# Kernel tuning notes

Hardware: AMD Instinct MI355X
Metric: run time of the kernel (lower is better)

## Reference

```python
import jax, jax.numpy as jnp
import numpy as np
from jax import lax

B, N, DIMS, CIN, K = 32, 1024, 3, 64, 16
COUTS = [128, 128, 128]
EPS = 1e-5


def knn_idx(points, k):
    # points: [B, D, N]; pairwise_distance = -||pi - pj||^2 (torch: -xx - (-2 p^T p) - xx^T)
    xx = jnp.sum(points ** 2, axis=1)                      # [B, N]
    inner = jnp.einsum('bdn,bdm->bnm', points, points)     # [B, N, N]
    pd = 2.0 * inner - xx[:, :, None] - xx[:, None, :]     # [B, N, N]
    idx = lax.top_k(pd, k + 1)[1][:, :, 1:]                # drop self -> [B, N, K]
    return idx


def batchnorm(x, gamma, beta, axes):
    # training-mode BN: biased batch statistics per channel (last axis here)
    mean = jnp.mean(x, axis=axes, keepdims=True)
    var = jnp.mean((x - mean) ** 2, axis=axes, keepdims=True)
    return (x - mean) * lax.rsqrt(var + EPS) * gamma + beta


def reference(points, features, W0, g0, b0, W1, g1, b1, W2, g2, b2, Wsc, gsc, bsc):
    idx = knn_idx(points, K)                               # [B, N, K] int32
    feats = jnp.transpose(features, (0, 2, 1))             # [B, N, C]
    nbr = jax.vmap(lambda f, i: f[i])(feats, idx)          # [B, N, K, C]
    center = feats[:, :, None, :]                          # [B, N, 1, C]
    # torch get_graph_feature: cat((x, fts - x), dim=channel) -> [B, N, K, 2C]
    x = jnp.concatenate([jnp.broadcast_to(center, nbr.shape), nbr - center], axis=-1)
    for W, g, b in ((W0, g0, b0), (W1, g1, b1), (W2, g2, b2)):
        x = jnp.einsum('bnkc,oc->bnko', x, W)              # 1x1 conv, no bias
        x = jax.nn.relu(batchnorm(x, g, b, axes=(0, 1, 2)))
    fts = jnp.mean(x, axis=2)                              # mean over neighbors -> [B, N, Co]
    sc = jnp.einsum('bnc,oc->bno', feats, Wsc)             # shortcut 1x1 conv1d
    sc = batchnorm(sc, gsc, bsc, axes=(0, 1))
    out = jax.nn.relu(sc + fts)                            # [B, N, Co]
    return jnp.transpose(out, (0, 2, 1))                   # [B, Co, N] to match torch layout


def setup_inputs() -> dict:
    key = jax.random.key(0)
    ks = jax.random.split(key, 8)
    s = 0.05
    return {
        'points': jax.random.normal(ks[0], (B, DIMS, N), jnp.float32),
        'features': jax.random.normal(ks[1], (B, CIN, N), jnp.float32),
        'W0': jax.random.normal(ks[2], (COUTS[0], 2 * CIN), jnp.float32) * s,
        'g0': jnp.ones((COUTS[0],), jnp.float32), 'b0': jnp.zeros((COUTS[0],), jnp.float32),
        'W1': jax.random.normal(ks[3], (COUTS[1], COUTS[0]), jnp.float32) * s,
        'g1': jnp.ones((COUTS[1],), jnp.float32), 'b1': jnp.zeros((COUTS[1],), jnp.float32),
        'W2': jax.random.normal(ks[4], (COUTS[2], COUTS[1]), jnp.float32) * s,
        'g2': jnp.ones((COUTS[2],), jnp.float32), 'b2': jnp.zeros((COUTS[2],), jnp.float32),
        'Wsc': jax.random.normal(ks[5], (COUTS[2], CIN), jnp.float32) * s,
        'gsc': jnp.ones((COUTS[2],), jnp.float32), 'bsc': jnp.zeros((COUTS[2],), jnp.float32),
    }
```

## Files before the change

kernel.cpp:

```cpp
#include <hip/hip_runtime.h>


#define BB 32
#define NN 1024
#define CINC 64
#define KK 16
#define CO 128
#define NROW (BB*NN*KK)
#define NROWSC (BB*NN)

static const size_t OFF_FT   = 0;
static const size_t OFF_IDX  = 8388608;
static const size_t OFF_Y    = 10485760;
static const size_t OFF_SC   = 144703488;
static const size_t OFF_PART = 161480704;
static const size_t OFF_WB   = 165675008;
static const size_t OFF_S1   = 169869312;
static const size_t OFF_SB   = 169934848;
static const size_t WS_NEED  = 169938944;

typedef __bf16 bf16x8v __attribute__((ext_vector_type(8)));
typedef float  f32x4v  __attribute__((ext_vector_type(4)));

__device__ __forceinline__ float bl(unsigned u){ return __uint_as_float(u<<16); }
__device__ __forceinline__ float bh(unsigned u){ return __uint_as_float(u & 0xffff0000u); }
__device__ __forceinline__ unsigned short bfr(float x){
  unsigned u = __float_as_uint(x);
  u += 0x7fffu + ((u>>16)&1u);
  return (unsigned short)(u>>16);
}
__device__ __forceinline__ unsigned short b16(float x){
  return __builtin_bit_cast(unsigned short, (__bf16)x);
}

__global__ __launch_bounds__(256) void sentinel_kernel(float* __restrict__ out, int n, float v){
  int i = blockIdx.x*256 + threadIdx.x;
  if (i < n) out[i] = v;
}

__global__ __launch_bounds__(256) void prep_kernel(const float* __restrict__ f,
                                                   const float* __restrict__ pts,
                                                   const float* __restrict__ W0,
                                                   const float* __restrict__ W1,
                                                   const float* __restrict__ W2,
                                                   float* __restrict__ ft,
                                                   unsigned short* __restrict__ WB,
                                                   int* __restrict__ idxout){
  __shared__ __align__(16) char smem[34816];
  int t = threadIdx.x;
  int bid = blockIdx.x;

  if (bid < 512){
    float (*tile)[65] = (float(*)[65])smem;
    int b = bid >> 4, n0 = (bid & 15) * 64;
    for (int it=0; it<16; ++it){
      int flat = it*256 + t;
      int c = flat>>6, nl = flat&63;
      tile[c][nl] = f[(b*64 + c)*1024 + n0 + nl];
    }
    __syncthreads();
    for (int it=0; it<16; ++it){
      int flat = it*256 + t;
      int nl = flat>>6, c = flat&63;
      ft[((b<<10) + n0 + nl)*64 + c] = tile[c][nl];
    }
    return;
  }

  if (bid < 536){
    int tid = (bid - 512)*256 + t;
    int lay = tid >> 11, rem = tid & 2047;
    int fidx = rem >> 6, l = rem & 63;
    int kb = fidx >> 3, cf = fidx & 7;
    int li = l & 15, lg = l >> 4;
    const float* Ws = lay==0 ? W0 : (lay==1 ? W1 : W2);
    int o = cf*16 + li;
    unsigned short p[8];
    #pragma unroll
    for (int j=0;j<8;++j) p[j] = bfr(Ws[o*128 + kb*32 + lg*8 + j]);
    uint4 o4;
    o4.x = (unsigned)p[0] | ((unsigned)p[1]<<16);
    o4.y = (unsigned)p[2] | ((unsigned)p[3]<<16);
    o4.z = (unsigned)p[4] | ((unsigned)p[5]<<16);
    o4.w = (unsigned)p[6] | ((unsigned)p[7]<<16);
    *reinterpret_cast<uint4*>(WB + (size_t)lay*16384 + (size_t)rem*8) = o4;
    return;
  }

  {
    int kbid = bid - 536;
    int b = kbid >> 5, g = kbid & 31;
    float4* p4 = (float4*)smem;
    unsigned long long (*mk)[32][17] =
        (unsigned long long(*)[32][17])smem;

    for (int i=t; i<1024; i+=256){
      float a = pts[(b*3+0)*1024+i];
      float c = pts[(b*3+1)*1024+i];
      float d = pts[(b*3+2)*1024+i];
      float xx = __fadd_rn(__fadd_rn(__fmul_rn(a,a), __fmul_rn(c,c)), __fmul_rn(d,d));
      p4[i] = make_float4(a, c, d, xx);
    }
    __syncthreads();

    int q = t & 31, c = t >> 5;
    int n = g*32 + q;
    float4 qp = p4[n];
    float qx=qp.x, qy=qp.y, qz=qp.z, qxx=qp.w;
    double vals[16];
    #pragma unroll
    for (int j=0;j<16;++j) vals[j] = 0.0;

    int m0 = c*128;
    for (int i0=0; i0<128; i0+=4){
      float4 cand[4];
      #pragma unroll
      for (int u=0;u<4;++u) cand[u] = p4[m0 + i0 + u];
      #pragma unroll
      for (int u=0;u<4;++u){
        int m = m0 + i0 + u;
        float inner = __fadd_rn(__fadd_rn(__fmul_rn(qx,cand[u].x), __fmul_rn(qy,cand[u].y)), __fmul_rn(qz,cand[u].z));
        float pd = __fsub_rn(__fsub_rn(__fmul_rn(2.0f, inner), qxx), cand[u].w);
        unsigned uv = __float_as_uint(pd);
        unsigned fk = uv ^ (0x80000000u | (unsigned)((int)uv >> 31));
        unsigned lo = (fk << 20) | (unsigned)(1023 - m);
        unsigned hi = 0x40000000u | (fk >> 12);
        hi = (m == n) ? 0u : hi;
        double key = __builtin_bit_cast(double, ((unsigned long long)hi << 32) | lo);
        #pragma unroll
        for (int j=0;j<16;++j){
          double mx = fmax(vals[j], key);
          key = fmin(vals[j], key);
          vals[j] = mx;
        }
      }
    }
    __syncthreads();
    #pragma unroll
    for (int j=0;j<16;++j) mk[c][q][j] = __builtin_bit_cast(unsigned long long, vals[j]);
    mk[c][q][16] = 0ull;
    __syncthreads();

    if (t < 32){
      int qq = t;
      int p0=0,p1=0,p2=0,p3=0,p4i=0,p5=0,p6=0,p7=0;
      unsigned long long v0=mk[0][qq][0], v1=mk[1][qq][0], v2=mk[2][qq][0], v3=mk[3][qq][0];
      unsigned long long v4=mk[4][qq][0], v5=mk[5][qq][0], v6=mk[6][qq][0], v7=mk[7][qq][0];
      int* dst = idxout + ((size_t)((b<<10) + g*32 + qq))*16;
      #pragma unroll
      for (int j=0;j<16;++j){
        unsigned long long best = v0; int bc = 0;
        if (v1 > best){ best = v1; bc = 1; }
        if (v2 > best){ best = v2; bc = 2; }
        if (v3 > best){ best = v3; bc = 3; }
        if (v4 > best){ best = v4; bc = 4; }
        if (v5 > best){ best = v5; bc = 5; }
        if (v6 > best){ best = v6; bc = 6; }
        if (v7 > best){ best = v7; bc = 7; }
        dst[j] = 1023 - (int)(best & 1023ull);
        if      (bc==0){ ++p0; v0 = mk[0][qq][p0]; }
        else if (bc==1){ ++p1; v1 = mk[1][qq][p1]; }
        else if (bc==2){ ++p2; v2 = mk[2][qq][p2]; }
        else if (bc==3){ ++p3; v3 = mk[3][qq][p3]; }
        else if (bc==4){ ++p4i; v4 = mk[4][qq][p4i]; }
        else if (bc==5){ ++p5; v5 = mk[5][qq][p5]; }
        else if (bc==6){ ++p6; v6 = mk[6][qq][p6]; }
        else           { ++p7; v7 = mk[7][qq][p7]; }
      }
    }
  }
}

template<int MODE>
__global__ __launch_bounds__(256, 2) void gemm4(const float* __restrict__ featsT,
                                                const int* __restrict__ knnidx,
                                                const unsigned short* yin,
                                                const float* __restrict__ sb,
                                                const unsigned short* __restrict__ Wswz,
                                                unsigned short* yout,
                                                float* __restrict__ partials){
  __shared__ __align__(16) unsigned short Wl[16384];
  __shared__ __align__(16) unsigned short tb[4][16][132];
  float* red = (float*)&tb[0][0][0];

  int t = threadIdx.x;
  int w = t >> 6, l = t & 63;
  int li = l & 15, lg = l >> 4;

  #pragma unroll
  for (int it=0; it<8; ++it){
    int v = it*256 + t;
    *reinterpret_cast<uint4*>(&Wl[v*8]) =
      *reinterpret_cast<const uint4*>(Wswz + (size_t)v*8);
  }
  __syncthreads();

  float ss[8] = {0.f,0.f,0.f,0.f,0.f,0.f,0.f,0.f};
  float sq[8] = {0.f,0.f,0.f,0.f,0.f,0.f,0.f,0.f};

  auto epilogue = [&](int rg, f32x4v (&acc)[8]){
    size_t rbase = (size_t)blockIdx.x*256 + w*64 + rg*16;
    #pragma unroll
    for (int cf=0; cf<8; ++cf){
      ss[cf] += acc[cf][0]+acc[cf][1]+acc[cf][2]+acc[cf][3];
      sq[cf] += acc[cf][0]*acc[cf][0]+acc[cf][1]*acc[cf][1]+acc[cf][2]*acc[cf][2]+acc[cf][3]*acc[cf][3];
    }
    #pragma unroll
    for (int cf=0; cf<8; ++cf){
      tb[w][lg*4 + 0][cf*16 + li] = b16(acc[cf][0]);
      tb[w][lg*4 + 1][cf*16 + li] = b16(acc[cf][1]);
      tb[w][lg*4 + 2][cf*16 + li] = b16(acc[cf][2]);
      tb[w][lg*4 + 3][cf*16 + li] = b16(acc[cf][3]);
    }
    __builtin_amdgcn_wave_barrier();
    {
      int row4 = l >> 4, ch = l & 15;
      #pragma unroll
      for (int s2=0; s2<4; ++s2){
        const unsigned short* src = &tb[w][s2*4 + row4][ch*8];
        unsigned short* dst = yout + (rbase + s2*4 + row4)*128 + ch*8;
        *reinterpret_cast<uint4*>(dst) = *reinterpret_cast<const uint4*>(src);
      }
    }
    __builtin_amdgcn_wave_barrier();
  };

  if constexpr (MODE == 1){
    const unsigned short* ybase = yin + ((size_t)blockIdx.x*256 + w*64 + li)*128 + lg*8;
    uint4 yb[2][4];
    #pragma unroll
    for (int kb=0; kb<4; ++kb)
      yb[0][kb] = *reinterpret_cast<const uint4*>(ybase + kb*32);
    #pragma unroll
    for (int rg=0; rg<4; ++rg){
      if (rg < 3){
        #pragma unroll
        for (int kb=0; kb<4; ++kb)
          yb[(rg+1)&1][kb] = *reinterpret_cast<const uint4*>(ybase + (size_t)(rg+1)*2048 + kb*32);
      }
      f32x4v acc[8] = {};
      #pragma unroll
      for (int kb=0; kb<4; ++kb){
        int c0 = kb*32 + lg*8;
        uint4 yv = yb[rg&1][kb];
        float4 s0 = *reinterpret_cast<const float4*>(sb + c0);
        float4 s1 = *reinterpret_cast<const float4*>(sb + c0 + 4);
        float4 b0 = *reinterpret_cast<const float4*>(sb + 128 + c0);
        float4 b1 = *reinterpret_cast<const float4*>(sb + 128 + c0 + 4);
        bf16x8v av;
        av[0] = (__bf16)fmaxf(fmaf(bl(yv.x), s0.x, b0.x), 0.f);
        av[1] = (__bf16)fmaxf(fmaf(bh(yv.x), s0.y, b0.y), 0.f);
        av[2] = (__bf16)fmaxf(fmaf(bl(yv.y), s0.z, b0.z), 0.f);
        av[3] = (__bf16)fmaxf(fmaf(bh(yv.y), s0.w, b0.w), 0.f);
        av[4] = (__bf16)fmaxf(fmaf(bl(yv.z), s1.x, b1.x), 0.f);
        av[5] = (__bf16)fmaxf(fmaf(bh(yv.z), s1.y, b1.y), 0.f);
        av[6] = (__bf16)fmaxf(fmaf(bl(yv.w), s1.z, b1.z), 0.f);
        av[7] = (__bf16)fmaxf(fmaf(bh(yv.w), s1.w, b1.w), 0.f);
        #pragma unroll
        for (int cf=0; cf<8; ++cf){
          uint4 b4 = *reinterpret_cast<const uint4*>(&Wl[((kb*8+cf)*64 + l)*8]);
          acc[cf] = __builtin_amdgcn_mfma_f32_16x16x32_bf16(av, __builtin_bit_cast(bf16x8v, b4), acc[cf], 0, 0, 0);
        }
      }
      epilogue(rg, acc);
    }
  } else {
    int b = blockIdx.x >> 6;
    int nbase = (blockIdx.x & 63)*16 + w*4;
    const float* fb = featsT + (((size_t)b)<<10)*64;
    int nbr[4];
    #pragma unroll
    for (int rg=0; rg<4; ++rg)
      nbr[rg] = knnidx[((size_t)((b<<10) + nbase + rg))*16 + li];
    float4 cg[2][4], ng[2][4];
    {
      const float* cp = fb + (size_t)nbase*64 + lg*8;
      const float* np = fb + (size_t)nbr[0]*64 + lg*8;
      cg[0][0] = *reinterpret_cast<const float4*>(cp);
      cg[0][1] = *reinterpret_cast<const float4*>(cp + 4);
      cg[0][2] = *reinterpret_cast<const float4*>(cp + 32);
      cg[0][3] = *reinterpret_cast<const float4*>(cp + 36);
      ng[0][0] = *reinterpret_cast<const float4*>(np);
      ng[0][1] = *reinterpret_cast<const float4*>(np + 4);
      ng[0][2] = *reinterpret_cast<const float4*>(np + 32);
      ng[0][3] = *reinterpret_cast<const float4*>(np + 36);
    }
    #pragma unroll
    for (int rg=0; rg<4; ++rg){
      if (rg < 3){
        const float* cp = fb + (size_t)(nbase + rg + 1)*64 + lg*8;
        const float* np = fb + (size_t)nbr[rg+1]*64 + lg*8;
        cg[(rg+1)&1][0] = *reinterpret_cast<const float4*>(cp);
        cg[(rg+1)&1][1] = *reinterpret_cast<const float4*>(cp + 4);
        cg[(rg+1)&1][2] = *reinterpret_cast<const float4*>(cp + 32);
        cg[(rg+1)&1][3] = *reinterpret_cast<const float4*>(cp + 36);
        ng[(rg+1)&1][0] = *reinterpret_cast<const float4*>(np);
        ng[(rg+1)&1][1] = *reinterpret_cast<const float4*>(np + 4);
        ng[(rg+1)&1][2] = *reinterpret_cast<const float4*>(np + 32);
        ng[(rg+1)&1][3] = *reinterpret_cast<const float4*>(np + 36);
      }
      float4 cl0 = cg[rg&1][0], cl1 = cg[rg&1][1], ch0 = cg[rg&1][2], ch1 = cg[rg&1][3];
      float4 nl0 = ng[rg&1][0], nl1 = ng[rg&1][1], nh0 = ng[rg&1][2], nh1 = ng[rg&1][3];
      bf16x8v afr[4];
      afr[0][0]=(__bf16)cl0.x; afr[0][1]=(__bf16)cl0.y; afr[0][2]=(__bf16)cl0.z; afr[0][3]=(__bf16)cl0.w;
      afr[0][4]=(__bf16)cl1.x; afr[0][5]=(__bf16)cl1.y; afr[0][6]=(__bf16)cl1.z; afr[0][7]=(__bf16)cl1.w;
      afr[1][0]=(__bf16)ch0.x; afr[1][1]=(__bf16)ch0.y; afr[1][2]=(__bf16)ch0.z; afr[1][3]=(__bf16)ch0.w;
      afr[1][4]=(__bf16)ch1.x; afr[1][5]=(__bf16)ch1.y; afr[1][6]=(__bf16)ch1.z; afr[1][7]=(__bf16)ch1.w;
      afr[2][0]=(__bf16)(nl0.x-cl0.x); afr[2][1]=(__bf16)(nl0.y-cl0.y);
      afr[2][2]=(__bf16)(nl0.z-cl0.z); afr[2][3]=(__bf16)(nl0.w-cl0.w);
      afr[2][4]=(__bf16)(nl1.x-cl1.x); afr[2][5]=(__bf16)(nl1.y-cl1.y);
      afr[2][6]=(__bf16)(nl1.z-cl1.z); afr[2][7]=(__bf16)(nl1.w-cl1.w);
      afr[3][0]=(__bf16)(nh0.x-ch0.x); afr[3][1]=(__bf16)(nh0.y-ch0.y);
      afr[3][2]=(__bf16)(nh0.z-ch0.z); afr[3][3]=(__bf16)(nh0.w-ch0.w);
      afr[3][4]=(__bf16)(nh1.x-ch1.x); afr[3][5]=(__bf16)(nh1.y-ch1.y);
      afr[3][6]=(__bf16)(nh1.z-ch1.z); afr[3][7]=(__bf16)(nh1.w-ch1.w);
      f32x4v acc[8] = {};
      #pragma unroll
      for (int kb=0; kb<4; ++kb){
        #pragma unroll
        for (int cf=0; cf<8; ++cf){
          uint4 b4 = *reinterpret_cast<const uint4*>(&Wl[((kb*8+cf)*64 + l)*8]);
          acc[cf] = __builtin_amdgcn_mfma_f32_16x16x32_bf16(afr[kb], __builtin_bit_cast(bf16x8v, b4), acc[cf], 0, 0, 0);
        }
      }
      epilogue(rg, acc);
    }
  }

  __syncthreads();
  #pragma unroll
  for (int cf=0; cf<8; ++cf){
    float s = ss[cf];
    s += __shfl_xor(s, 16);
    s += __shfl_xor(s, 32);
    float q = sq[cf];
    q += __shfl_xor(q, 16);
    q += __shfl_xor(q, 32);
    if (lg == 0){
      red[w*128 + cf*16 + li]       = s;
      red[512 + w*128 + cf*16 + li] = q;
    }
  }
  __syncthreads();
  {
    int col = t & 127;
    int base = (t >> 7) * 512;
    float s = red[base + col] + red[base + 128 + col] + red[base + 256 + col] + red[base + 384 + col];
    partials[(size_t)blockIdx.x*256 + (t>>7)*128 + col] = s;
  }
}

__global__ __launch_bounds__(256) void sc_gemm(const float* __restrict__ featsT,
                                               const float* __restrict__ W,
                                               float* __restrict__ scout,
                                               float* __restrict__ partials){
  __shared__ __align__(16) unsigned short Wt[64][136];
  __shared__ __align__(16) unsigned short xs[64][72];
  int t = threadIdx.x, tx = t&15, ty = t>>4;
  int rowbase = blockIdx.x * 64;
  for (int it=0; it<32; ++it){
    int flat = it*256 + t;
    int o = flat>>6, c = flat&63;
    Wt[c][o] = bfr(W[flat]);
  }
  for (int it=0; it<16; ++it){
    int flat = it*256 + t;
    int r = flat>>6, c = flat&63;
    xs[r][c] = bfr(featsT[(size_t)(rowbase + r)*64 + c]);
  }
  __syncthreads();
  float acc[4][8] = {};
  for (int c=0;c<64;++c){
    uint4 wv = *reinterpret_cast<const uint4*>(&Wt[c][tx*8]);
    float w[8];
    w[0]=bl(wv.x); w[1]=bh(wv.x); w[2]=bl(wv.y); w[3]=bh(wv.y);
    w[4]=bl(wv.z); w[5]=bh(wv.z); w[6]=bl(wv.w); w[7]=bh(wv.w);
    #pragma unroll
    for (int i=0;i<4;++i){
      float xv = bl((unsigned)xs[ty*4+i][c]);
      #pragma unroll
      for (int j=0;j<8;++j) acc[i][j] = fmaf(xv, w[j], acc[i][j]);
    }
  }
  #pragma unroll
  for (int i=0;i<4;++i)
    #pragma unroll
    for (int j=0;j<8;++j)
      scout[(size_t)(rowbase + ty*4 + i)*128 + tx*8 + j] = acc[i][j];

  __syncthreads();
  float* red = reinterpret_cast<float*>(&xs[0][0]);
  #pragma unroll
  for (int j=0;j<8;++j){
    float s=0.f;
    #pragma unroll
    for (int i=0;i<4;++i) s += acc[i][j];
    red[ty*128 + tx*8 + j] = s;
  }
  __syncthreads();
  if (t<128){
    float s=0.f;
    for (int y2=0;y2<16;++y2) s += red[y2*128 + t];
    partials[(size_t)blockIdx.x*256 + t] = s;
  }
  __syncthreads();
  #pragma unroll
  for (int j=0;j<8;++j){
    float s=0.f;
    #pragma unroll
    for (int i=0;i<4;++i) s += acc[i][j]*acc[i][j];
    red[ty*128 + tx*8 + j] = s;
  }
  __syncthreads();
  if (t<128){
    float s=0.f;
    for (int y2=0;y2<16;++y2) s += red[y2*128 + t];
    partials[(size_t)blockIdx.x*256 + 128 + t] = s;
  }
}

__global__ __launch_bounds__(256) void bn_stats(const float* __restrict__ partials,
                                                int rows, float inv_count,
                                                const float* __restrict__ g,
                                                const float* __restrict__ beta,
                                                float* __restrict__ sbout){
  __shared__ float red[512];
  int c = blockIdx.x;
  int t = threadIdx.x;
  float s = 0.f, q = 0.f;
  for (int r = t; r < rows; r += 256){
    s += partials[(size_t)r*256 + c];
    q += partials[(size_t)r*256 + 128 + c];
  }
  red[t] = s; red[256 + t] = q;
  __syncthreads();
  #pragma unroll
  for (int off = 128; off > 0; off >>= 1){
    if (t < off){
      red[t]       += red[t + off];
      red[256 + t] += red[256 + t + off];
    }
    __syncthreads();
  }
  if (t == 0){
    float mean = red[0] * inv_count;
    float var  = fmaxf(red[256] * inv_count - mean*mean, 0.f);
    float rstd = 1.0f / sqrtf(var + 1e-5f);
    float sc = g[c] * rstd;
    sbout[c] = sc;
    sbout[128 + c] = beta[c] - mean*sc;
  }
}

__global__ __launch_bounds__(256) void final_kernel(const unsigned short* __restrict__ y2,
                                                    const float* __restrict__ sc,
                                                    const float* __restrict__ sb2,
                                                    const float* __restrict__ sbsc,
                                                    float* __restrict__ out){
  __shared__ __align__(16) float obuf[64][130];
  int t = threadIdx.x;
  int b = blockIdx.x >> 4;
  int n0 = (blockIdx.x & 15) * 64;
  int oc = (t & 15) * 8;
  int nl0 = t >> 4;

  float4 s2a = *reinterpret_cast<const float4*>(sb2 + oc);
  float4 s2b = *reinterpret_cast<const float4*>(sb2 + oc + 4);
  float4 c2a = *reinterpret_cast<const float4*>(sb2 + 128 + oc);
  float4 c2b = *reinterpret_cast<const float4*>(sb2 + 128 + oc + 4);
  float4 ssa = *reinterpret_cast<const float4*>(sbsc + oc);
  float4 ssb = *reinterpret_cast<const float4*>(sbsc + oc + 4);
  float4 csa = *reinterpret_cast<const float4*>(sbsc + 128 + oc);
  float4 csb = *reinterpret_cast<const float4*>(sbsc + 128 + oc + 4);

  #pragma unroll
  for (int p=0; p<4; ++p){
    int nl = p*16 + nl0;
    size_t nglob = (size_t)((b<<10) + n0 + nl);
    const unsigned short* yp = y2 + (nglob<<4)*128 + oc;
    float a0=0,a1=0,a2=0,a3=0,a4=0,a5=0,a6=0,a7=0;
    #pragma unroll
    for (int k=0;k<16;++k){
      uint4 v = *reinterpret_cast<const uint4*>(yp + k*128);
      a0 += fmaxf(fmaf(bl(v.x), s2a.x, c2a.x), 0.f);
      a1 += fmaxf(fmaf(bh(v.x), s2a.y, c2a.y), 0.f);
      a2 += fmaxf(fmaf(bl(v.y), s2a.z, c2a.z), 0.f);
      a3 += fmaxf(fmaf(bh(v.y), s2a.w, c2a.w), 0.f);
      a4 += fmaxf(fmaf(bl(v.z), s2b.x, c2b.x), 0.f);
      a5 += fmaxf(fmaf(bh(v.z), s2b.y, c2b.y), 0.f);
      a6 += fmaxf(fmaf(bl(v.w), s2b.z, c2b.z), 0.f);
      a7 += fmaxf(fmaf(bh(v.w), s2b.w, c2b.w), 0.f);
    }
    const float* scp = sc + nglob*128 + oc;
    float4 v0 = *reinterpret_cast<const float4*>(scp);
    float4 v1 = *reinterpret_cast<const float4*>(scp + 4);
    float4 o0, o1;
    o0.x = fmaxf(fmaf(v0.x, ssa.x, csa.x) + a0*(1.f/16.f), 0.f);
    o0.y = fmaxf(fmaf(v0.y, ssa.y, csa.y) + a1*(1.f/16.f), 0.f);
    o0.z = fmaxf(fmaf(v0.z, ssa.z, csa.z) + a2*(1.f/16.f), 0.f);
    o0.w = fmaxf(fmaf(v0.w, ssa.w, csa.w) + a3*(1.f/16.f), 0.f);
    o1.x = fmaxf(fmaf(v1.x, ssb.x, csb.x) + a4*(1.f/16.f), 0.f);
    o1.y = fmaxf(fmaf(v1.y, ssb.y, csb.y) + a5*(1.f/16.f), 0.f);
    o1.z = fmaxf(fmaf(v1.z, ssb.z, csb.z) + a6*(1.f/16.f), 0.f);
    o1.w = fmaxf(fmaf(v1.w, ssb.w, csb.w) + a7*(1.f/16.f), 0.f);
    *reinterpret_cast<float4*>(&obuf[nl][oc])     = o0;
    *reinterpret_cast<float4*>(&obuf[nl][oc + 4]) = o1;
  }
  __syncthreads();
  for (int it=0; it<32; ++it){
    int flat = it*256 + t;
    int oo = flat>>6, nl = flat&63;
    out[((size_t)b<<17) + (oo<<10) + n0 + nl] = obuf[nl][oo];
  }
}

extern "C" void kernel_launch(void* const* d_in, const int* in_sizes, int n_in,
                              void* d_out, int out_size, void* d_ws, size_t ws_size,
                              hipStream_t stream) {
  const float* points   = (const float*)d_in[0];
  const float* features = (const float*)d_in[1];
  const float* W0  = (const float*)d_in[2];
  const float* g0  = (const float*)d_in[3];
  const float* b0  = (const float*)d_in[4];
  const float* W1  = (const float*)d_in[5];
  const float* g1  = (const float*)d_in[6];
  const float* b1  = (const float*)d_in[7];
  const float* W2  = (const float*)d_in[8];
  const float* g2  = (const float*)d_in[9];
  const float* b2  = (const float*)d_in[10];
  const float* Wsc = (const float*)d_in[11];
  const float* gsc = (const float*)d_in[12];
  const float* bsc = (const float*)d_in[13];

  float* out = (float*)d_out;

  if (ws_size < WS_NEED){
    float v = (float)(ws_size >> 20);
    sentinel_kernel<<<(out_size + 255)/256, 256, 0, stream>>>(out, out_size, v);
    return;
  }

  char* ws = (char*)d_ws;
  float*          featsT = (float*)(ws + OFF_FT);
  int*            idx    = (int*)(ws + OFF_IDX);
  unsigned short* y      = (unsigned short*)(ws + OFF_Y);
  float*          scbuf  = (float*)(ws + OFF_SC);
  float*          part   = (float*)(ws + OFF_PART);
  unsigned short* WB     = (unsigned short*)(ws + OFF_WB);
  float*          sb     = (float*)(ws + OFF_SB);

  prep_kernel<<<1560, 256, 0, stream>>>(features, points, W0, W1, W2, featsT, WB, idx);

  gemm4<0><<<NROW/256, 256, 0, stream>>>(featsT, idx, nullptr, nullptr, WB, y, part);
  bn_stats<<<128, 256, 0, stream>>>(part, 2048, 1.f/524288.f, g0, b0, sb + 0);
  gemm4<1><<<NROW/256, 256, 0, stream>>>(nullptr, nullptr, y, sb + 0, WB + 16384, y, part);
  bn_stats<<<128, 256, 0, stream>>>(part, 2048, 1.f/524288.f, g1, b1, sb + 256);
  gemm4<1><<<NROW/256, 256, 0, stream>>>(nullptr, nullptr, y, sb + 256, WB + 32768, y, part);
  bn_stats<<<128, 256, 0, stream>>>(part, 2048, 1.f/524288.f, g2, b2, sb + 512);
  sc_gemm<<<NROWSC/64, 256, 0, stream>>>(featsT, Wsc, scbuf, part);
  bn_stats<<<128, 256, 0, stream>>>(part, 512, 1.f/32768.f, gsc, bsc, sb + 768);
  final_kernel<<<512, 256, 0, stream>>>(y, scbuf, sb + 512, sb + 768, out);
}
```

Measured before the change: 305.4 us.

## Fold shortcut GEMM into prep kernel and merge its BN stats with layer 0

Result: faster. 290.7 us, median of 2 (-4.8%).

```diff
diff --git a/kernel.cpp b/kernel.cpp
--- a/kernel.cpp
+++ b/kernel.cpp
@@ -14,8 +14,8 @@
 static const size_t OFF_Y    = 10485760;
 static const size_t OFF_SC   = 144703488;
 static const size_t OFF_PART = 161480704;
+static const size_t OFF_PART2= 163577856;
 static const size_t OFF_WB   = 165675008;
-static const size_t OFF_S1   = 169869312;
 static const size_t OFF_SB   = 169934848;
 static const size_t WS_NEED  = 169938944;
 
@@ -43,9 +43,12 @@
                                                    const float* __restrict__ W0,
                                                    const float* __restrict__ W1,
                                                    const float* __restrict__ W2,
+                                                   const float* __restrict__ Wsc,
                                                    float* __restrict__ ft,
                                                    unsigned short* __restrict__ WB,
-                                                   int* __restrict__ idxout){
+                                                   int* __restrict__ idxout,
+                                                   float* __restrict__ scout,
+                                                   float* __restrict__ part2){
   __shared__ __align__(16) char smem[34816];
   int t = threadIdx.x;
   int bid = blockIdx.x;
@@ -87,7 +90,7 @@
     return;
   }
 
-  {
+  if (bid < 1560){
     int kbid = bid - 536;
     int b = kbid >> 5, g = kbid & 31;
     float4* p4 = (float4*)smem;
@@ -167,6 +170,76 @@
         else if (bc==6){ ++p6; v6 = mk[6][qq][p6]; }
         else           { ++p7; v7 = mk[7][qq][p7]; }
       }
+    }
+    return;
+  }
+
+  {
+    int scb = bid - 1560;
+    int rowbase = scb * 64;
+    int b = rowbase >> 10, n0 = rowbase & 1023;
+    unsigned short (*Wt)[136] = (unsigned short(*)[136])smem;
+    unsigned short (*xs)[72]  = (unsigned short(*)[72])(smem + 17408);
+    float* red = (float*)(smem + 17408);
+    int tx = t & 15, ty = t >> 4;
+
+    for (int it=0; it<32; ++it){
+      int flat = it*256 + t;
+      int o = flat>>6, c = flat&63;
+      Wt[c][o] = bfr(Wsc[flat]);
+    }
+    for (int it=0; it<16; ++it){
+      int flat = it*256 + t;
+      int c = flat>>6, nl = flat&63;
+      xs[nl][c] = bfr(f[(b*64 + c)*1024 + n0 + nl]);
+    }
+    __syncthreads();
+    float acc[4][8] = {};
+    for (int c=0;c<64;++c){
+      uint4 wv = *reinterpret_cast<const uint4*>(&Wt[c][tx*8]);
+      float w[8];
+      w[0]=bl(wv.x); w[1]=bh(wv.x); w[2]=bl(wv.y); w[3]=bh(wv.y);
+      w[4]=bl(wv.z); w[5]=bh(wv.z); w[6]=bl(wv.w); w[7]=bh(wv.w);
+      #pragma unroll
+      for (int i=0;i<4;++i){
+        float xv = bl((unsigned)xs[ty*4+i][c]);
+        #pragma unroll
+        for (int j=0;j<8;++j) acc[i][j] = fmaf(xv, w[j], acc[i][j]);
+      }
+    }
+    #pragma unroll
+    for (int i=0;i<4;++i)
+      #pragma unroll
+      for (int j=0;j<8;++j)
+        scout[(size_t)(rowbase + ty*4 + i)*128 + tx*8 + j] = acc[i][j];
+
+    __syncthreads();
+    #pragma unroll
+    for (int j=0;j<8;++j){
+      float s=0.f;
+      #pragma unroll
+      for (int i=0;i<4;++i) s += acc[i][j];
+      red[ty*128 + tx*8 + j] = s;
+    }
+    __syncthreads();
+    if (t<128){
+      float s=0.f;
+      for (int y2=0;y2<16;++y2) s += red[y2*128 + t];
+      part2[(size_t)scb*256 + t] = s;
+    }
+    __syncthreads();
+    #pragma unroll
+    for (int j=0;j<8;++j){
+      float s=0.f;
+      #pragma unroll
+      for (int i=0;i<4;++i) s += acc[i][j]*acc[i][j];
+      red[ty*128 + tx*8 + j] = s;
+    }
+    __syncthreads();
+    if (t<128){
+      float s=0.f;
+      for (int y2=0;y2<16;++y2) s += red[y2*128 + t];
+      part2[(size_t)scb*256 + 128 + t] = s;
     }
   }
 }
@@ -350,75 +423,6 @@
   }
 }
 
-__global__ __launch_bounds__(256) void sc_gemm(const float* __restrict__ featsT,
-                                               const float* __restrict__ W,
-                                               float* __restrict__ scout,
-                                               float* __restrict__ partials){
-  __shared__ __align__(16) unsigned short Wt[64][136];
-  __shared__ __align__(16) unsigned short xs[64][72];
-  int t = threadIdx.x, tx = t&15, ty = t>>4;
-  int rowbase = blockIdx.x * 64;
-  for (int it=0; it<32; ++it){
-    int flat = it*256 + t;
-    int o = flat>>6, c = flat&63;
-    Wt[c][o] = bfr(W[flat]);
-  }
-  for (int it=0; it<16; ++it){
-    int flat = it*256 + t;
-    int r = flat>>6, c = flat&63;
-    xs[r][c] = bfr(featsT[(size_t)(rowbase + r)*64 + c]);
-  }
-  __syncthreads();
-  float acc[4][8] = {};
-  for (int c=0;c<64;++c){
-    uint4 wv = *reinterpret_cast<const uint4*>(&Wt[c][tx*8]);
-    float w[8];
-    w[0]=bl(wv.x); w[1]=bh(wv.x); w[2]=bl(wv.y); w[3]=bh(wv.y);
-    w[4]=bl(wv.z); w[5]=bh(wv.z); w[6]=bl(wv.w); w[7]=bh(wv.w);
-    #pragma unroll
-    for (int i=0;i<4;++i){
-      float xv = bl((unsigned)xs[ty*4+i][c]);
-      #pragma unroll
-      for (int j=0;j<8;++j) acc[i][j] = fmaf(xv, w[j], acc[i][j]);
-    }
-  }
-  #pragma unroll
-  for (int i=0;i<4;++i)
-    #pragma unroll
-    for (int j=0;j<8;++j)
-      scout[(size_t)(rowbase + ty*4 + i)*128 + tx*8 + j] = acc[i][j];
-
-  __syncthreads();
-  float* red = reinterpret_cast<float*>(&xs[0][0]);
-  #pragma unroll
-  for (int j=0;j<8;++j){
-    float s=0.f;
-    #pragma unroll
-    for (int i=0;i<4;++i) s += acc[i][j];
-    red[ty*128 + tx*8 + j] = s;
-  }
-  __syncthreads();
-  if (t<128){
-    float s=0.f;
-    for (int y2=0;y2<16;++y2) s += red[y2*128 + t];
-    partials[(size_t)blockIdx.x*256 + t] = s;
-  }
-  __syncthreads();
-  #pragma unroll
-  for (int j=0;j<8;++j){
-    float s=0.f;
-    #pragma unroll
-    for (int i=0;i<4;++i) s += acc[i][j]*acc[i][j];
-    red[ty*128 + tx*8 + j] = s;
-  }
-  __syncthreads();
-  if (t<128){
-    float s=0.f;
-    for (int y2=0;y2<16;++y2) s += red[y2*128 + t];
-    partials[(size_t)blockIdx.x*256 + 128 + t] = s;
-  }
-}
-
 __global__ __launch_bounds__(256) void bn_stats(const float* __restrict__ partials,
                                                 int rows, float inv_count,
                                                 const float* __restrict__ g,
@@ -449,6 +453,45 @@
     float sc = g[c] * rstd;
     sbout[c] = sc;
     sbout[128 + c] = beta[c] - mean*sc;
+  }
+}
+
+__global__ __launch_bounds__(256) void bn_stats2(const float* __restrict__ partA,
+                                                 const float* __restrict__ partB,
+                                                 const float* __restrict__ gA,
+                                                 const float* __restrict__ bA,
+                                                 const float* __restrict__ gB,
+                                                 const float* __restrict__ bB,
+                                                 float* __restrict__ outA,
+                                                 float* __restrict__ outB){
+  __shared__ float red[512];
+  int blk = blockIdx.x;
+  int t = threadIdx.x;
+  const float* part; int rows; float inv; const float* g; const float* be; float* o; int c;
+  if (blk < 128){ part = partA; rows = 2048; inv = 1.f/524288.f; g = gA; be = bA; o = outA; c = blk; }
+  else          { part = partB; rows = 512;  inv = 1.f/32768.f;  g = gB; be = bB; o = outB; c = blk - 128; }
+  float s = 0.f, q = 0.f;
+  for (int r = t; r < rows; r += 256){
+    s += part[(size_t)r*256 + c];
+    q += part[(size_t)r*256 + 128 + c];
+  }
+  red[t] = s; red[256 + t] = q;
+  __syncthreads();
+  #pragma unroll
+  for (int off = 128; off > 0; off >>= 1){
+    if (t < off){
+      red[t]       += red[t + off];
+      red[256 + t] += red[256 + t + off];
+    }
+    __syncthreads();
+  }
+  if (t == 0){
+    float mean = red[0] * inv;
+    float var  = fmaxf(red[256] * inv - mean*mean, 0.f);
+    float rstd = 1.0f / sqrtf(var + 1e-5f);
+    float sc = g[c] * rstd;
+    o[c] = sc;
+    o[128 + c] = be[c] - mean*sc;
   }
 }
 
@@ -546,18 +589,18 @@
   unsigned short* y      = (unsigned short*)(ws + OFF_Y);
   float*          scbuf  = (float*)(ws + OFF_SC);
   float*          part   = (float*)(ws + OFF_PART);
+  float*          part2  = (float*)(ws + OFF_PART2);
   unsigned short* WB     = (unsigned short*)(ws + OFF_WB);
   float*          sb     = (float*)(ws + OFF_SB);
 
-  prep_kernel<<<1560, 256, 0, stream>>>(features, points, W0, W1, W2, featsT, WB, idx);
+  prep_kernel<<<2072, 256, 0, stream>>>(features, points, W0, W1, W2, Wsc,
+                                        featsT, WB, idx, scbuf, part2);
 
   gemm4<0><<<NROW/256, 256, 0, stream>>>(featsT, idx, nullptr, nullptr, WB, y, part);
-  bn_stats<<<128, 256, 0, stream>>>(part, 2048, 1.f/524288.f, g0, b0, sb + 0);
+  bn_stats2<<<256, 256, 0, stream>>>(part, part2, g0, b0, gsc, bsc, sb + 0, sb + 768);
   gemm4<1><<<NROW/256, 256, 0, stream>>>(nullptr, nullptr, y, sb + 0, WB + 16384, y, part);
   bn_stats<<<128, 256, 0, stream>>>(part, 2048, 1.f/524288.f, g1, b1, sb + 256);
   gemm4<1><<<NROW/256, 256, 0, stream>>>(nullptr, nullptr, y, sb + 256, WB + 32768, y, part);
   bn_stats<<<128, 256, 0, stream>>>(part, 2048, 1.f/524288.f, g2, b2, sb + 512);
-  sc_gemm<<<NROWSC/64, 256, 0, stream>>>(featsT, Wsc, scbuf, part);
-  bn_stats<<<128, 256, 0, stream>>>(part, 512, 1.f/32768.f, gsc, bsc, sb + 768);
   final_kernel<<<512, 256, 0, stream>>>(y, scbuf, sb + 512, sb + 768, out);
 }
```
